# Kernel tuning notes

Hardware: AMD Instinct MI355X
Metric: run time of the kernel (lower is better)

## Reference

```python
import jax, jax.numpy as jnp
import numpy as np

C = 256
C8 = C // 8


def setup_inputs() -> dict:
    key = jax.random.key(0)
    ks = jax.random.split(key, 9)
    B, H, W = 4, 64, 64
    inp = jax.random.normal(ks[0], (B, C, H, W), dtype=jnp.float32)
    original = jax.random.normal(ks[1], (B, C, H, W), dtype=jnp.float32)
    s = 1.0 / np.sqrt(C)
    wq = jax.random.normal(ks[2], (C8, C), dtype=jnp.float32) * s
    bq = jax.random.normal(ks[3], (C8,), dtype=jnp.float32) * 0.01
    wk = jax.random.normal(ks[4], (C8, C), dtype=jnp.float32) * s
    bk = jax.random.normal(ks[5], (C8,), dtype=jnp.float32) * 0.01
    wv = jax.random.normal(ks[6], (C, C), dtype=jnp.float32) * s
    bv = jax.random.normal(ks[7], (C,), dtype=jnp.float32) * 0.01
    # torch inits gamma to 0; use a nonzero value so the attention branch contributes
    gamma = jnp.asarray([0.5], dtype=jnp.float32)
    return {"input": inp, "original": original, "wq": wq, "bq": bq,
            "wk": wk, "bk": bk, "wv": wv, "bv": bv, "gamma": gamma}


def reference(input, original, wq, bq, wk, bk, wv, bv, gamma):
    B, Cc, H, W = input.shape
    HW = H * W
    x = input.reshape(B, Cc, HW)          # [B, C, HW]
    o = original.reshape(B, Cc, HW)
    # 1x1 convs == per-pixel linear projections
    q = jnp.einsum('oc,bcn->bno', wq, x) + bq          # [B, HW, C8]
    k = jnp.einsum('oc,bcn->bon', wk, x) + bk[:, None]  # [B, C8, HW]
    v = jnp.einsum('oc,bcn->bon', wv, o) + bv[:, None]  # [B, C, HW]
    attn = jax.nn.softmax(jnp.einsum('bic,bcj->bij', q, k), axis=-1)  # [B, HW, HW]
    out = jnp.einsum('bcj,bij->bci', v, attn)           # [B, C, HW]
    out = out.reshape(B, Cc, H, W)
    return gamma[0] * out + input
```

## Files before the change

### kernel.cpp

```cpp
#include <hip/hip_runtime.h>

typedef short s16x8 __attribute__((ext_vector_type(8)));
typedef float f32x4 __attribute__((ext_vector_type(4)));
typedef float f32x16 __attribute__((ext_vector_type(16)));

#define B_ 4
#define C_ 256
#define S_ 4096
#define LOG2E 1.44269504088896f
#define M2 32.0f

#if __has_builtin(__builtin_amdgcn_exp2f)
#define EXP2(x) __builtin_amdgcn_exp2f(x)
#else
#define EXP2(x) __exp2f(x)
#endif

__device__ __forceinline__ unsigned short f2b(float f) {
  union { float f; unsigned u; } v; v.f = f;
  unsigned r = v.u + 0x7fffu + ((v.u >> 16) & 1u);
  return (unsigned short)(r >> 16);
}
__device__ __forceinline__ unsigned short f2b_fast(float f) {
  union { float f; unsigned u; } v; v.f = f;
  return (unsigned short)((v.u + 0x8000u) >> 16);
}
#define PK2(x, y) ((unsigned)f2b_fast(x) | ((unsigned)f2b_fast(y) << 16))
__device__ __forceinline__ s16x8 lds_ld8(const unsigned short* p) {
  union { s16x8 v; uint2 u[2]; } r;
  r.u[0] = *(const uint2*)p;
  r.u[1] = *(const uint2*)(p + 4);
  return r.v;
}

__global__ __launch_bounds__(256)
void proj_kernel(const float* __restrict__ x, const float* __restrict__ orig,
                 const float* __restrict__ wq, const float* __restrict__ bq,
                 const float* __restrict__ wk, const float* __restrict__ bk,
                 const float* __restrict__ wv, const float* __restrict__ bv,
                 unsigned short* __restrict__ Qb, unsigned short* __restrict__ Kb,
                 unsigned short* __restrict__ Vf) {
  __shared__ unsigned short Al[64 * 68];
  __shared__ unsigned short Sl[64 * 68];
  const int ct = blockIdx.x >> 6;
  const int jt = blockIdx.x & 63;
  const int n0 = jt * 64;
  const int b  = blockIdx.y;
  const int t  = threadIdx.x;
  const int L = t & 63, w = t >> 6;
  const int mt = w >> 1, nt = w & 1;
  const int g = L >> 5, l32 = L & 31;
  const float* srcb = ((ct == 0) ? x : orig) + (size_t)b * C_ * S_;
  f32x16 acc = (f32x16)0.0f;

  for (int kc = 0; kc < 4; ++kc) {
    const int k0 = kc * 64;
    __syncthreads();
    #pragma unroll
    for (int rep = 0; rep < 4; ++rep) {
      const int idx = rep * 256 + t;
      const int row = idx >> 4, c4 = (idx & 15) * 4;
      const float* wsrc; int wrow;
      if (ct == 0) {
        if (row < 32) { wsrc = wq; wrow = row; } else { wsrc = wk; wrow = row - 32; }
      } else { wsrc = wv; wrow = (ct - 1) * 64 + row; }
      f32x4 v = *(const f32x4*)(wsrc + (size_t)wrow * 256 + k0 + c4);
      union { unsigned short us[4]; uint2 u2; } pk;
      #pragma unroll
      for (int i = 0; i < 4; ++i) pk.us[i] = f2b(v[i]);
      *(uint2*)&Al[row * 68 + c4] = pk.u2;
    }
    {
      const int c4 = (t >> 4) * 4;
      const int n4 = (t & 15) * 4;
      f32x4 v0 = *(const f32x4*)(srcb + (size_t)(k0 + c4 + 0) * S_ + n0 + n4);
      f32x4 v1 = *(const f32x4*)(srcb + (size_t)(k0 + c4 + 1) * S_ + n0 + n4);
      f32x4 v2 = *(const f32x4*)(srcb + (size_t)(k0 + c4 + 2) * S_ + n0 + n4);
      f32x4 v3 = *(const f32x4*)(srcb + (size_t)(k0 + c4 + 3) * S_ + n0 + n4);
      #pragma unroll
      for (int k = 0; k < 4; ++k) {
        union { unsigned short us[4]; uint2 u2; } pk;
        pk.us[0] = f2b(v0[k]); pk.us[1] = f2b(v1[k]);
        pk.us[2] = f2b(v2[k]); pk.us[3] = f2b(v3[k]);
        *(uint2*)&Sl[(n4 + k) * 68 + c4] = pk.u2;
      }
    }
    __syncthreads();
    #pragma unroll
    for (int ks = 0; ks < 4; ++ks) {
      s16x8 af = lds_ld8(&Al[(mt * 32 + l32) * 68 + ks * 16 + g * 8]);
      s16x8 bf = lds_ld8(&Sl[(nt * 32 + l32) * 68 + ks * 16 + g * 8]);
      acc = __builtin_amdgcn_mfma_f32_32x32x16_bf16(af, bf, acc, 0, 0, 0);
    }
  }
  __syncthreads();
  unsigned short* Rl = Al;
  const int n = nt * 32 + l32;
  if (ct == 0) {
    #pragma unroll
    for (int reg = 0; reg < 16; ++reg) {
      const int rr = (reg & 3) + 8 * (reg >> 2) + 4 * g;
      const float val = (mt == 0) ? (acc[reg] + bq[rr]) * LOG2E : acc[reg] + bk[rr];
      Rl[n * 68 + mt * 32 + rr] = f2b(val);
    }
    __syncthreads();
    const int nn = t >> 2, ch0 = (t & 3) * 16;
    s16x8 a = lds_ld8(Rl + nn * 68 + ch0);
    s16x8 c = lds_ld8(Rl + nn * 68 + ch0 + 8);
    unsigned short* dst = (ch0 < 32)
        ? Qb + ((size_t)b * S_ + n0 + nn) * 32 + ch0
        : Kb + ((size_t)b * S_ + n0 + nn) * 32 + (ch0 - 32);
    *(s16x8*)dst = a;
    *(s16x8*)(dst + 8) = c;
  } else {
    const int cg = ct - 1;
    #pragma unroll
    for (int reg = 0; reg < 16; ++reg) {
      const int rr = (reg & 3) + 8 * (reg >> 2) + 4 * g;
      const int ch = mt * 32 + rr;
      Rl[ch * 68 + n] = f2b(acc[reg] + bv[cg * 64 + ch]);
    }
    __syncthreads();
    #pragma unroll
    for (int k = 0; k < 2; ++k) {
      const int G = t * 2 + k;
      const int t2 = G >> 8;
      const int gh = (G >> 7) & 1;
      const int s  = (G >> 6) & 1;
      const int Lf = G & 63;
      const int hh = Lf >> 5;
      const int ch_l = gh * 32 + (Lf & 31);
      const int jloc = t2 * 32 + s * 16 + hh * 4;
      uint2 q0 = *(const uint2*)&Rl[ch_l * 68 + jloc];
      uint2 q1 = *(const uint2*)&Rl[ch_l * 68 + jloc + 8];
      unsigned short* dst = Vf + (((size_t)(b * 128 + jt * 2 + t2) * 8)
                                  + cg * 2 + gh) * 1024 + s * 512 + (size_t)Lf * 8;
      *(uint2*)dst = q0;
      *(uint2*)(dst + 4) = q1;
    }
  }
}


#define MFMA32(A, B, C) __builtin_amdgcn_mfma_f32_32x32x16_bf16(A, B, C, 0, 0, 0)

#define LOADV(JT)                                                               \
  {                                                                             \
    const unsigned short* vb = Vf + (((size_t)(b * 128 + (JT)) * 8)             \
                                     + chh * 4) * 1024 + (size_t)L * 8;         \
    v00 = *(const s16x8*)(vb + 0 * 1024);                                       \
    v01 = *(const s16x8*)(vb + 0 * 1024 + 512);                                 \
    v10 = *(const s16x8*)(vb + 1 * 1024);                                       \
    v11 = *(const s16x8*)(vb + 1 * 1024 + 512);                                 \
    v20 = *(const s16x8*)(vb + 2 * 1024);                                       \
    v21 = *(const s16x8*)(vb + 2 * 1024 + 512);                                 \
    v30 = *(const s16x8*)(vb + 3 * 1024);                                       \
    v31 = *(const s16x8*)(vb + 3 * 1024 + 512);                                 \
  }

__global__ __launch_bounds__(256, 3)
void flash_kernel(const unsigned short* __restrict__ Qb,
                  const unsigned short* __restrict__ Kb,
                  const unsigned short* __restrict__ Vf,
                  const float* __restrict__ inp,
                  const float* __restrict__ gamma,
                  float* __restrict__ out) {
  __shared__ float scr[32][260];
  __shared__ float lpart[2][32];
  __shared__ float invl[32];
  const int l  = blockIdx.x;
  const int b  = (l & 7) >> 1;
  const int i0 = ((l >> 3) * 2 + (l & 1)) * 32;
  const int t  = threadIdx.x;
  const int L = t & 63, w = t >> 6;
  const int l31 = L & 31, h = L >> 5;
  const int jq = w & 1, chh = w >> 1;
  const float gam = gamma[0];
  const unsigned short* Kbase = Kb + (size_t)b * S_ * 32;

  {
    float* sf = &scr[0][0];
    for (int z = t; z < 32 * 260; z += 256) sf[z] = 0.0f;
  }

  const s16x8 qf0 = *(const s16x8*)(Qb + ((size_t)b * S_ + i0 + l31) * 32 + h * 8);
  const s16x8 qf1 = *(const s16x8*)(Qb + ((size_t)b * S_ + i0 + l31) * 32 + 16 + h * 8);

  f32x16 a0 = (f32x16)0.0f, a1 = (f32x16)0.0f, a2 = (f32x16)0.0f, a3 = (f32x16)0.0f;
  float lpv = 0.f;
  const f32x16 cinit = (f32x16)(-M2);

  s16x8 kc0, kc1, kn0, kn1;
  s16x8 v00, v01, v10, v11, v20, v21, v30, v31;
  {
    const int jt0 = jq * 64;
    kc0 = *(const s16x8*)(Kbase + (size_t)(jt0 * 32 + l31) * 32 + h * 8);
    kc1 = *(const s16x8*)(Kbase + (size_t)(jt0 * 32 + l31) * 32 + 16 + h * 8);
  }

  for (int st = 0; st < 64; ++st) {
    const int jt = jq * 64 + st;
    LOADV(jt);
    {
      const int jn = (st < 63) ? jt + 1 : jt;
      kn0 = *(const s16x8*)(Kbase + (size_t)(jn * 32 + l31) * 32 + h * 8);
      kn1 = *(const s16x8*)(Kbase + (size_t)(jn * 32 + l31) * 32 + 16 + h * 8);
    }
    f32x16 p = MFMA32(kc0, qf0, cinit);
    p = MFMA32(kc1, qf1, p);
    const float e0 = EXP2(p[0]),  e1 = EXP2(p[1]),  e2 = EXP2(p[2]),  e3 = EXP2(p[3]);
    const float e4 = EXP2(p[4]),  e5 = EXP2(p[5]),  e6 = EXP2(p[6]),  e7 = EXP2(p[7]);
    const float e8 = EXP2(p[8]),  e9 = EXP2(p[9]),  e10 = EXP2(p[10]), e11 = EXP2(p[11]);
    const float e12 = EXP2(p[12]), e13 = EXP2(p[13]), e14 = EXP2(p[14]), e15 = EXP2(p[15]);
    lpv += (((e0 + e1) + (e2 + e3)) + ((e4 + e5) + (e6 + e7)))
         + (((e8 + e9) + (e10 + e11)) + ((e12 + e13) + (e14 + e15)));
    union { unsigned u[4]; s16x8 v; } pa, pb;
    pa.u[0] = PK2(e0, e1);   pa.u[1] = PK2(e2, e3);
    pa.u[2] = PK2(e4, e5);   pa.u[3] = PK2(e6, e7);
    pb.u[0] = PK2(e8, e9);   pb.u[1] = PK2(e10, e11);
    pb.u[2] = PK2(e12, e13); pb.u[3] = PK2(e14, e15);
    a0 = MFMA32(pa.v, v00, a0);  a0 = MFMA32(pb.v, v01, a0);
    a1 = MFMA32(pa.v, v10, a1);  a1 = MFMA32(pb.v, v11, a1);
    a2 = MFMA32(pa.v, v20, a2);  a2 = MFMA32(pb.v, v21, a2);
    a3 = MFMA32(pa.v, v30, a3);  a3 = MFMA32(pb.v, v31, a3);
    kc0 = kn0; kc1 = kn1;
  }

  lpv += __shfl_xor(lpv, 32, 64);
  if (chh == 0 && L < 32) lpart[jq][L] = lpv;
  #pragma unroll 1
  for (int ph = 0; ph < 2; ++ph) {
    __syncthreads();
    if (jq == ph) {
      #pragma unroll
      for (int r = 0; r < 16; ++r) {
        const int rr = (r & 3) + 8 * (r >> 2) + 4 * h;
        scr[rr][chh * 128 + 0 * 32 + l31] += a0[r];
        scr[rr][chh * 128 + 1 * 32 + l31] += a1[r];
        scr[rr][chh * 128 + 2 * 32 + l31] += a2[r];
        scr[rr][chh * 128 + 3 * 32 + l31] += a3[r];
      }
    }
  }
  __syncthreads();
  if (t < 32) invl[t] = gam / (lpart[0][t] + lpart[1][t]);
  __syncthreads();
  {
    const int chq = t >> 3;
    const int i4  = (t & 7) * 4;
    #pragma unroll
    for (int cc = 0; cc < 8; ++cc) {
      const int ch = cc * 32 + chq;
      const size_t gi = ((size_t)b * C_ + ch) * S_ + i0 + i4;
      const f32x4 iv = *(const f32x4*)(inp + gi);
      f32x4 o;
      #pragma unroll
      for (int k = 0; k < 4; ++k)
        o[k] = scr[i4 + k][ch] * invl[i4 + k] + iv[k];
      *(f32x4*)(out + gi) = o;
    }
  }
}

extern "C" void kernel_launch(void* const* d_in, const int* in_sizes, int n_in,
                              void* d_out, int out_size, void* d_ws, size_t ws_size,
                              hipStream_t stream) {
  const float* inp   = (const float*)d_in[0];
  const float* orig  = (const float*)d_in[1];
  const float* wq    = (const float*)d_in[2];
  const float* bq    = (const float*)d_in[3];
  const float* wk    = (const float*)d_in[4];
  const float* bk    = (const float*)d_in[5];
  const float* wv    = (const float*)d_in[6];
  const float* bv    = (const float*)d_in[7];
  const float* gamma = (const float*)d_in[8];
  float* out = (float*)d_out;

  unsigned short* Qb = (unsigned short*)d_ws;
  unsigned short* Kb = Qb + (size_t)B_ * S_ * 32;
  unsigned short* Vf = Kb + (size_t)B_ * S_ * 32;

  proj_kernel<<<dim3(320, 4), 256, 0, stream>>>(inp, orig, wq, bq, wk, bk, wv, bv, Qb, Kb, Vf);
  flash_kernel<<<512, 256, 0, stream>>>(Qb, Kb, Vf, inp, gamma, out);
}
```

Measured before the change: 161.8 us.

## Enlarge flash tile to 64 queries per block with 512 threads and 4-way key split

Each block now handles 64 query rows across 8 waves: two query groups by four key quarters, where before it handled 32 rows across 4 waves. Every wave computes all 256 output channels, loading V in two halves per key tile and keeping eight accumulators. Each V tile loaded from global memory is now reused across 64 query rows instead of 32, which halves V traffic per query. The cost is more accumulator registers per wave, fewer blocks (256) on the device, and a four-phase serialized shared-memory reduction with a larger LDS footprint.

```diff
diff --git a/kernel.cpp b/kernel.cpp
--- a/kernel.cpp
+++ b/kernel.cpp
@@ -144,70 +144,84 @@
 
 #define MFMA32(A, B, C) __builtin_amdgcn_mfma_f32_32x32x16_bf16(A, B, C, 0, 0, 0)
 
-#define LOADV(JT)                                                               \
+#define LOADV_H(JT, HF)                                                         \
   {                                                                             \
     const unsigned short* vb = Vf + (((size_t)(b * 128 + (JT)) * 8)             \
-                                     + chh * 4) * 1024 + (size_t)L * 8;         \
-    v00 = *(const s16x8*)(vb + 0 * 1024);                                       \
-    v01 = *(const s16x8*)(vb + 0 * 1024 + 512);                                 \
-    v10 = *(const s16x8*)(vb + 1 * 1024);                                       \
-    v11 = *(const s16x8*)(vb + 1 * 1024 + 512);                                 \
-    v20 = *(const s16x8*)(vb + 2 * 1024);                                       \
-    v21 = *(const s16x8*)(vb + 2 * 1024 + 512);                                 \
-    v30 = *(const s16x8*)(vb + 3 * 1024);                                       \
-    v31 = *(const s16x8*)(vb + 3 * 1024 + 512);                                 \
-  }
-
-__global__ __launch_bounds__(256, 3)
+                                     + (HF) * 4) * 1024 + (size_t)L * 8;        \
+    v0 = *(const s16x8*)(vb + 0 * 1024);                                        \
+    v1 = *(const s16x8*)(vb + 0 * 1024 + 512);                                  \
+    v2 = *(const s16x8*)(vb + 1 * 1024);                                        \
+    v3 = *(const s16x8*)(vb + 1 * 1024 + 512);                                  \
+    v4 = *(const s16x8*)(vb + 2 * 1024);                                        \
+    v5 = *(const s16x8*)(vb + 2 * 1024 + 512);                                  \
+    v6 = *(const s16x8*)(vb + 3 * 1024);                                        \
+    v7 = *(const s16x8*)(vb + 3 * 1024 + 512);                                  \
+  }
+
+#define PV_H(A0, A1, A2, A3)                                                    \
+  A0 = MFMA32(pa.v, v0, A0);  A0 = MFMA32(pb.v, v1, A0);                        \
+  A1 = MFMA32(pa.v, v2, A1);  A1 = MFMA32(pb.v, v3, A1);                        \
+  A2 = MFMA32(pa.v, v4, A2);  A2 = MFMA32(pb.v, v5, A2);                        \
+  A3 = MFMA32(pa.v, v6, A3);  A3 = MFMA32(pb.v, v7, A3);
+
+#define DUMP_ADD(ACC, CG)                                                       \
+  _Pragma("unroll")                                                             \
+  for (int r = 0; r < 16; ++r) {                                                \
+    const int rr = (r & 3) + 8 * (r >> 2) + 4 * h;                              \
+    scr[ig * 32 + rr][(CG) * 32 + l31] += ACC[r];                               \
+  }
+
+__global__ __launch_bounds__(512, 2)
 void flash_kernel(const unsigned short* __restrict__ Qb,
                   const unsigned short* __restrict__ Kb,
                   const unsigned short* __restrict__ Vf,
                   const float* __restrict__ inp,
                   const float* __restrict__ gamma,
                   float* __restrict__ out) {
-  __shared__ float scr[32][260];
-  __shared__ float lpart[2][32];
-  __shared__ float invl[32];
+  __shared__ float scr[64][260];
+  __shared__ float lpart[4][64];
+  __shared__ float invl[64];
   const int l  = blockIdx.x;
   const int b  = (l & 7) >> 1;
-  const int i0 = ((l >> 3) * 2 + (l & 1)) * 32;
+  const int i0 = ((l >> 3) * 2 + (l & 1)) * 64;
   const int t  = threadIdx.x;
   const int L = t & 63, w = t >> 6;
   const int l31 = L & 31, h = L >> 5;
-  const int jq = w & 1, chh = w >> 1;
+  const int ig = w & 1, jq = w >> 1;
   const float gam = gamma[0];
   const unsigned short* Kbase = Kb + (size_t)b * S_ * 32;
 
   {
     float* sf = &scr[0][0];
-    for (int z = t; z < 32 * 260; z += 256) sf[z] = 0.0f;
-  }
-
-  const s16x8 qf0 = *(const s16x8*)(Qb + ((size_t)b * S_ + i0 + l31) * 32 + h * 8);
-  const s16x8 qf1 = *(const s16x8*)(Qb + ((size_t)b * S_ + i0 + l31) * 32 + 16 + h * 8);
+    for (int z = t; z < 64 * 260; z += 512) sf[z] = 0.0f;
+  }
+
+  const s16x8 qf0 = *(const s16x8*)(Qb + ((size_t)b * S_ + i0 + ig * 32 + l31) * 32 + h * 8);
+  const s16x8 qf1 = *(const s16x8*)(Qb + ((size_t)b * S_ + i0 + ig * 32 + l31) * 32 + 16 + h * 8);
 
   f32x16 a0 = (f32x16)0.0f, a1 = (f32x16)0.0f, a2 = (f32x16)0.0f, a3 = (f32x16)0.0f;
+  f32x16 a4 = (f32x16)0.0f, a5 = (f32x16)0.0f, a6 = (f32x16)0.0f, a7 = (f32x16)0.0f;
   float lpv = 0.f;
   const f32x16 cinit = (f32x16)(-M2);
 
   s16x8 kc0, kc1, kn0, kn1;
-  s16x8 v00, v01, v10, v11, v20, v21, v30, v31;
+  s16x8 v0, v1, v2, v3, v4, v5, v6, v7;
   {
-    const int jt0 = jq * 64;
+    const int jt0 = jq * 32;
     kc0 = *(const s16x8*)(Kbase + (size_t)(jt0 * 32 + l31) * 32 + h * 8);
     kc1 = *(const s16x8*)(Kbase + (size_t)(jt0 * 32 + l31) * 32 + 16 + h * 8);
   }
 
-  for (int st = 0; st < 64; ++st) {
-    const int jt = jq * 64 + st;
-    LOADV(jt);
+  for (int st = 0; st < 32; ++st) {
+    const int jt = jq * 32 + st;
+    LOADV_H(jt, 0);
+    f32x16 p = MFMA32(kc0, qf0, cinit);
+    p = MFMA32(kc1, qf1, p);
     {
-      const int jn = (st < 63) ? jt + 1 : jt;
+      const int jn = (st < 31) ? jt + 1 : jt;
       kn0 = *(const s16x8*)(Kbase + (size_t)(jn * 32 + l31) * 32 + h * 8);
       kn1 = *(const s16x8*)(Kbase + (size_t)(jn * 32 + l31) * 32 + 16 + h * 8);
     }
-    f32x16 p = MFMA32(kc0, qf0, cinit);
-    p = MFMA32(kc1, qf1, p);
     const float e0 = EXP2(p[0]),  e1 = EXP2(p[1]),  e2 = EXP2(p[2]),  e3 = EXP2(p[3]);
     const float e4 = EXP2(p[4]),  e5 = EXP2(p[5]),  e6 = EXP2(p[6]),  e7 = EXP2(p[7]);
     const float e8 = EXP2(p[8]),  e9 = EXP2(p[9]),  e10 = EXP2(p[10]), e11 = EXP2(p[11]);
@@ -219,44 +233,37 @@
     pa.u[2] = PK2(e4, e5);   pa.u[3] = PK2(e6, e7);
     pb.u[0] = PK2(e8, e9);   pb.u[1] = PK2(e10, e11);
     pb.u[2] = PK2(e12, e13); pb.u[3] = PK2(e14, e15);
-    a0 = MFMA32(pa.v, v00, a0);  a0 = MFMA32(pb.v, v01, a0);
-    a1 = MFMA32(pa.v, v10, a1);  a1 = MFMA32(pb.v, v11, a1);
-    a2 = MFMA32(pa.v, v20, a2);  a2 = MFMA32(pb.v, v21, a2);
-    a3 = MFMA32(pa.v, v30, a3);  a3 = MFMA32(pb.v, v31, a3);
+    PV_H(a0, a1, a2, a3);
+    LOADV_H(jt, 1);
+    PV_H(a4, a5, a6, a7);
     kc0 = kn0; kc1 = kn1;
   }
 
   lpv += __shfl_xor(lpv, 32, 64);
-  if (chh == 0 && L < 32) lpart[jq][L] = lpv;
+  if (L < 32) lpart[jq][ig * 32 + L] = lpv;
   #pragma unroll 1
-  for (int ph = 0; ph < 2; ++ph) {
+  for (int ph = 0; ph < 4; ++ph) {
     __syncthreads();
     if (jq == ph) {
-      #pragma unroll
-      for (int r = 0; r < 16; ++r) {
-        const int rr = (r & 3) + 8 * (r >> 2) + 4 * h;
-        scr[rr][chh * 128 + 0 * 32 + l31] += a0[r];
-        scr[rr][chh * 128 + 1 * 32 + l31] += a1[r];
-        scr[rr][chh * 128 + 2 * 32 + l31] += a2[r];
-        scr[rr][chh * 128 + 3 * 32 + l31] += a3[r];
-      }
+      DUMP_ADD(a0, 0); DUMP_ADD(a1, 1); DUMP_ADD(a2, 2); DUMP_ADD(a3, 3);
+      DUMP_ADD(a4, 4); DUMP_ADD(a5, 5); DUMP_ADD(a6, 6); DUMP_ADD(a7, 7);
     }
   }
   __syncthreads();
-  if (t < 32) invl[t] = gam / (lpart[0][t] + lpart[1][t]);
+  if (t < 64) invl[t] = gam / (lpart[0][t] + lpart[1][t] + lpart[2][t] + lpart[3][t]);
   __syncthreads();
   {
-    const int chq = t >> 3;
-    const int i4  = (t & 7) * 4;
-    #pragma unroll
-    for (int cc = 0; cc < 8; ++cc) {
-      const int ch = cc * 32 + chq;
-      const size_t gi = ((size_t)b * C_ + ch) * S_ + i0 + i4;
+    const int ch = t >> 1;
+    const int ih = (t & 1) * 32;
+    #pragma unroll
+    for (int q = 0; q < 8; ++q) {
+      const int il = ih + q * 4;
+      const size_t gi = ((size_t)b * C_ + ch) * S_ + i0 + il;
       const f32x4 iv = *(const f32x4*)(inp + gi);
       f32x4 o;
       #pragma unroll
       for (int k = 0; k < 4; ++k)
-        o[k] = scr[i4 + k][ch] * invl[i4 + k] + iv[k];
+        o[k] = scr[il + k][ch] * invl[il + k] + iv[k];
       *(f32x4*)(out + gi) = o;
     }
   }
@@ -281,5 +288,5 @@
   unsigned short* Vf = Kb + (size_t)B_ * S_ * 32;
 
   proj_kernel<<<dim3(320, 4), 256, 0, stream>>>(inp, orig, wq, bq, wk, bk, wv, bv, Qb, Kb, Vf);
-  flash_kernel<<<512, 256, 0, stream>>>(Qb, Kb, Vf, inp, gamma, out);
-}
+  flash_kernel<<<256, 512, 0, stream>>>(Qb, Kb, Vf, inp, gamma, out);
+}
```

Result: faster. 154.2 us (-4.7%).

## Split key range across six wave groups with 768-thread flash blocks

Applied to the files above, without the earlier changes.

Each flash block grows from 4 to 12 waves. The key range is split into six slices instead of two, so each wave handles about a third as many key tiles and the per-block critical path gets shorter. The slices are merged through six serialized LDS accumulation phases, and the epilogue store mapping is rewritten for 512 threads. The risks are more barriers and phases, higher register pressure from launch_bounds(768,3), and fewer blocks resident per CU.

```diff
diff --git a/kernel.cpp b/kernel.cpp
--- a/kernel.cpp
+++ b/kernel.cpp
@@ -158,7 +158,7 @@
     v31 = *(const s16x8*)(vb + 3 * 1024 + 512);                                 \
   }
 
-__global__ __launch_bounds__(256, 3)
+__global__ __launch_bounds__(768, 3)
 void flash_kernel(const unsigned short* __restrict__ Qb,
                   const unsigned short* __restrict__ Kb,
                   const unsigned short* __restrict__ Vf,
@@ -166,7 +166,7 @@
                   const float* __restrict__ gamma,
                   float* __restrict__ out) {
   __shared__ float scr[32][260];
-  __shared__ float lpart[2][32];
+  __shared__ float lpart[6][32];
   __shared__ float invl[32];
   const int l  = blockIdx.x;
   const int b  = (l & 7) >> 1;
@@ -174,13 +174,16 @@
   const int t  = threadIdx.x;
   const int L = t & 63, w = t >> 6;
   const int l31 = L & 31, h = L >> 5;
-  const int jq = w & 1, chh = w >> 1;
+  const int chh = w & 1, js = w >> 1;
   const float gam = gamma[0];
   const unsigned short* Kbase = Kb + (size_t)b * S_ * 32;
 
+  const int jt_beg = (js * 128) / 6;
+  const int jt_end = ((js + 1) * 128) / 6;
+
   {
     float* sf = &scr[0][0];
-    for (int z = t; z < 32 * 260; z += 256) sf[z] = 0.0f;
+    for (int z = t; z < 32 * 260; z += 768) sf[z] = 0.0f;
   }
 
   const s16x8 qf0 = *(const s16x8*)(Qb + ((size_t)b * S_ + i0 + l31) * 32 + h * 8);
@@ -192,17 +195,13 @@
 
   s16x8 kc0, kc1, kn0, kn1;
   s16x8 v00, v01, v10, v11, v20, v21, v30, v31;
-  {
-    const int jt0 = jq * 64;
-    kc0 = *(const s16x8*)(Kbase + (size_t)(jt0 * 32 + l31) * 32 + h * 8);
-    kc1 = *(const s16x8*)(Kbase + (size_t)(jt0 * 32 + l31) * 32 + 16 + h * 8);
-  }
-
-  for (int st = 0; st < 64; ++st) {
-    const int jt = jq * 64 + st;
+  kc0 = *(const s16x8*)(Kbase + (size_t)(jt_beg * 32 + l31) * 32 + h * 8);
+  kc1 = *(const s16x8*)(Kbase + (size_t)(jt_beg * 32 + l31) * 32 + 16 + h * 8);
+
+  for (int jt = jt_beg; jt < jt_end; ++jt) {
     LOADV(jt);
     {
-      const int jn = (st < 63) ? jt + 1 : jt;
+      const int jn = (jt + 1 < jt_end) ? jt + 1 : jt;
       kn0 = *(const s16x8*)(Kbase + (size_t)(jn * 32 + l31) * 32 + h * 8);
       kn1 = *(const s16x8*)(Kbase + (size_t)(jn * 32 + l31) * 32 + 16 + h * 8);
     }
@@ -227,11 +226,11 @@
   }
 
   lpv += __shfl_xor(lpv, 32, 64);
-  if (chh == 0 && L < 32) lpart[jq][L] = lpv;
+  if (chh == 0 && L < 32) lpart[js][L] = lpv;
   #pragma unroll 1
-  for (int ph = 0; ph < 2; ++ph) {
-    __syncthreads();
-    if (jq == ph) {
+  for (int ph = 0; ph < 6; ++ph) {
+    __syncthreads();
+    if (js == ph) {
       #pragma unroll
       for (int r = 0; r < 16; ++r) {
         const int rr = (r & 3) + 8 * (r >> 2) + 4 * h;
@@ -243,20 +242,21 @@
     }
   }
   __syncthreads();
-  if (t < 32) invl[t] = gam / (lpart[0][t] + lpart[1][t]);
+  if (t < 32) invl[t] = gam / (lpart[0][t] + lpart[1][t] + lpart[2][t]
+                               + lpart[3][t] + lpart[4][t] + lpart[5][t]);
   __syncthreads();
-  {
-    const int chq = t >> 3;
-    const int i4  = (t & 7) * 4;
-    #pragma unroll
-    for (int cc = 0; cc < 8; ++cc) {
-      const int ch = cc * 32 + chq;
-      const size_t gi = ((size_t)b * C_ + ch) * S_ + i0 + i4;
+  if (t < 512) {
+    const int ch = t >> 1;
+    const int ih = (t & 1) * 16;
+    #pragma unroll
+    for (int q = 0; q < 4; ++q) {
+      const int il = ih + q * 4;
+      const size_t gi = ((size_t)b * C_ + ch) * S_ + i0 + il;
       const f32x4 iv = *(const f32x4*)(inp + gi);
       f32x4 o;
       #pragma unroll
       for (int k = 0; k < 4; ++k)
-        o[k] = scr[i4 + k][ch] * invl[i4 + k] + iv[k];
+        o[k] = scr[il + k][ch] * invl[il + k] + iv[k];
       *(f32x4*)(out + gi) = o;
     }
   }
@@ -281,5 +281,5 @@
   unsigned short* Vf = Kb + (size_t)B_ * S_ * 32;
 
   proj_kernel<<<dim3(320, 4), 256, 0, stream>>>(inp, orig, wq, bq, wk, bk, wv, bv, Qb, Kb, Vf);
-  flash_kernel<<<512, 256, 0, stream>>>(Qb, Kb, Vf, inp, gamma, out);
-}
+  flash_kernel<<<512, 768, 0, stream>>>(Qb, Kb, Vf, inp, gamma, out);
+}
```

After: 244.8 us. 51.3% more time.
